# Optimization experiments

Hardware: AMD Instinct MI355X
Metric: run time of the kernel (lower is better)

The kernel has to match this reference:

```python
import jax, jax.numpy as jnp
import numpy as np

EPS = 1e-9

def setup_inputs() -> dict:
    key = jax.random.key(0)
    k1, k2 = jax.random.split(key)
    B, D = 65536, 512
    e = jax.random.normal(k1, (B, D), dtype=jnp.float32)
    tau = jax.random.normal(k2, (B, D), dtype=jnp.float32)
    return {"e": e, "tau": tau}

def reference(e, tau):
    # Barlow Twins (diagonal-only) loss.
    # torch .std(dim=0) is unbiased (ddof=1).
    B = e.shape[0]
    e_norm = (e - e.mean(axis=0)) / (e.std(axis=0, ddof=1) + EPS)
    tau_norm = (tau - tau.mean(axis=0)) / (tau.std(axis=0, ddof=1) + EPS)
    # diag(e_norm.T @ tau_norm) / B == per-feature batch reduction of products
    c_diag = jnp.sum(e_norm * tau_norm, axis=0) / B
    return jnp.sum((1.0 - c_diag) ** 2)
```

## Files before the change

kernel.cpp:

```cpp
#include <hip/hip_runtime.h>

#define BT_D  512
#define BT_D4 128
#define NBLK  1024
#define NTHR  256
#define BT_U  8

#define BT_ACC(ev, tv)                                                  \
    do {                                                                \
        se.x += (ev).x; se.y += (ev).y; se.z += (ev).z; se.w += (ev).w; \
        st.x += (tv).x; st.y += (tv).y; st.z += (tv).z; st.w += (tv).w; \
        se2.x = fmaf((ev).x, (ev).x, se2.x);                            \
        se2.y = fmaf((ev).y, (ev).y, se2.y);                            \
        se2.z = fmaf((ev).z, (ev).z, se2.z);                            \
        se2.w = fmaf((ev).w, (ev).w, se2.w);                            \
        st2.x = fmaf((tv).x, (tv).x, st2.x);                            \
        st2.y = fmaf((tv).y, (tv).y, st2.y);                            \
        st2.z = fmaf((tv).z, (tv).z, st2.z);                            \
        st2.w = fmaf((tv).w, (tv).w, st2.w);                            \
        set.x = fmaf((ev).x, (tv).x, set.x);                            \
        set.y = fmaf((ev).y, (tv).y, set.y);                            \
        set.z = fmaf((ev).z, (tv).z, set.z);                            \
        set.w = fmaf((ev).w, (tv).w, set.w);                            \
    } while (0)

__global__ __launch_bounds__(NTHR, 4) void bt_partial_kernel(
    const float4* __restrict__ e4, const float4* __restrict__ t4,
    float* __restrict__ acc, int B, int nslot)
{
    const int tid = threadIdx.x;
    const int c4  = tid & (BT_D4 - 1);
    const int r   = tid >> 7;

    float4 se  = make_float4(0.f, 0.f, 0.f, 0.f);
    float4 se2 = make_float4(0.f, 0.f, 0.f, 0.f);
    float4 st  = make_float4(0.f, 0.f, 0.f, 0.f);
    float4 st2 = make_float4(0.f, 0.f, 0.f, 0.f);
    float4 set = make_float4(0.f, 0.f, 0.f, 0.f);

    const size_t T  = (size_t)gridDim.x * NTHR;
    const size_t N4 = (size_t)B * BT_D4;
    size_t i = (size_t)blockIdx.x * NTHR + tid;

    for (; i + (BT_U - 1) * T < N4; i += BT_U * T) {
        float4 ev[BT_U], tv[BT_U];
#pragma unroll
        for (int u = 0; u < BT_U; ++u) {
            ev[u] = e4[i + u * T];
            tv[u] = t4[i + u * T];
        }
#pragma unroll
        for (int u = 0; u < BT_U; ++u) BT_ACC(ev[u], tv[u]);
    }
    for (; i < N4; i += T) {
        const float4 ev = e4[i];
        const float4 tv = t4[i];
        BT_ACC(ev, tv);
    }

    __shared__ float4 lds[BT_D4][5];
    if (r == 1) {
        lds[c4][0] = se;  lds[c4][1] = se2; lds[c4][2] = st;
        lds[c4][3] = st2; lds[c4][4] = set;
    }
    __syncthreads();
    if (r == 0) {
        float4 a;
        a = lds[c4][0]; se.x += a.x; se.y += a.y; se.z += a.z; se.w += a.w;
        a = lds[c4][1]; se2.x += a.x; se2.y += a.y; se2.z += a.z; se2.w += a.w;
        a = lds[c4][2]; st.x += a.x; st.y += a.y; st.z += a.z; st.w += a.w;
        a = lds[c4][3]; st2.x += a.x; st2.y += a.y; st2.z += a.z; st2.w += a.w;
        a = lds[c4][4]; set.x += a.x; set.y += a.y; set.z += a.z; set.w += a.w;

        float* ap = acc + (size_t)(blockIdx.x % nslot) * (5 * BT_D);
        const int col = c4 * 4;
        atomicAdd(&ap[0 * BT_D + col + 0], se.x);
        atomicAdd(&ap[0 * BT_D + col + 1], se.y);
        atomicAdd(&ap[0 * BT_D + col + 2], se.z);
        atomicAdd(&ap[0 * BT_D + col + 3], se.w);
        atomicAdd(&ap[1 * BT_D + col + 0], se2.x);
        atomicAdd(&ap[1 * BT_D + col + 1], se2.y);
        atomicAdd(&ap[1 * BT_D + col + 2], se2.z);
        atomicAdd(&ap[1 * BT_D + col + 3], se2.w);
        atomicAdd(&ap[2 * BT_D + col + 0], st.x);
        atomicAdd(&ap[2 * BT_D + col + 1], st.y);
        atomicAdd(&ap[2 * BT_D + col + 2], st.z);
        atomicAdd(&ap[2 * BT_D + col + 3], st.w);
        atomicAdd(&ap[3 * BT_D + col + 0], st2.x);
        atomicAdd(&ap[3 * BT_D + col + 1], st2.y);
        atomicAdd(&ap[3 * BT_D + col + 2], st2.z);
        atomicAdd(&ap[3 * BT_D + col + 3], st2.w);
        atomicAdd(&ap[4 * BT_D + col + 0], set.x);
        atomicAdd(&ap[4 * BT_D + col + 1], set.y);
        atomicAdd(&ap[4 * BT_D + col + 2], set.z);
        atomicAdd(&ap[4 * BT_D + col + 3], set.w);
    }
}

__global__ __launch_bounds__(512) void bt_final_kernel(
    const float* __restrict__ acc, float* __restrict__ out, int B, int nslot)
{
    const int d = threadIdx.x;
    double Se = 0, Se2 = 0, St = 0, St2 = 0, Set = 0;
    for (int s = 0; s < nslot; ++s) {
        const float* a = acc + (size_t)s * (5 * BT_D);
        Se  += a[0 * BT_D + d];
        Se2 += a[1 * BT_D + d];
        St  += a[2 * BT_D + d];
        St2 += a[3 * BT_D + d];
        Set += a[4 * BT_D + d];
    }
    const double Bd = (double)B;
    const double me = Se / Bd, mt = St / Bd;
    double ve = (Se2 - Bd * me * me) / (Bd - 1.0);
    double vt = (St2 - Bd * mt * mt) / (Bd - 1.0);
    ve = ve > 0.0 ? ve : 0.0;
    vt = vt > 0.0 ? vt : 0.0;
    const double sd_e = sqrt(ve) + 1e-9;
    const double sd_t = sqrt(vt) + 1e-9;
    const double c = (Set - Bd * me * mt) / (sd_e * sd_t * Bd);
    const double v = (1.0 - c) * (1.0 - c);

    __shared__ double red[BT_D];
    red[d] = v;
    __syncthreads();
    for (int s = BT_D / 2; s > 0; s >>= 1) {
        if (d < s) red[d] += red[d + s];
        __syncthreads();
    }
    if (d == 0) out[0] = (float)red[0];
}

extern "C" void kernel_launch(void* const* d_in, const int* in_sizes, int n_in,
                              void* d_out, int out_size, void* d_ws, size_t ws_size,
                              hipStream_t stream) {
    const float* e   = (const float*)d_in[0];
    const float* tau = (const float*)d_in[1];
    const int B = in_sizes[0] / BT_D;
    float* acc = (float*)d_ws;

    int nslot = 1;
    const size_t slot_bytes = (size_t)5 * BT_D * sizeof(float);
    if (ws_size >= 32 * slot_bytes)      nslot = 32;
    else if (ws_size >= 8 * slot_bytes)  nslot = 8;
    else if (ws_size >= 4 * slot_bytes)  nslot = 4;
    else if (ws_size >= 2 * slot_bytes)  nslot = 2;

    (void)hipMemsetAsync(d_ws, 0, (size_t)nslot * slot_bytes, stream);

    bt_partial_kernel<<<NBLK, NTHR, 0, stream>>>(
        (const float4*)e, (const float4*)tau, acc, B, nslot);
    bt_final_kernel<<<1, BT_D, 0, stream>>>(acc, (float*)d_out, B, nslot);
}
```

Baseline: 291.5 us.

## Stream inputs through LDS with async global_load_lds pipeline per wave

Replaces the grid-stride register loads with a per-wave software pipeline that uses global_load_lds to prefetch four stages of e and tau rows into shared memory, tracked with manual vmcnt waits. Each wave owns a contiguous range of rows and one half of the feature columns, which changes the access pattern to contiguous chunks. The final kernel is also restructured to read float4 slots across four thread groups and accumulate in float before converting to double. This adds reliance on inline waitcnt counting and clamped redundant loads at range ends, and the float accumulation in the final kernel may reduce precision.

```diff
diff --git a/kernel.cpp b/kernel.cpp
--- a/kernel.cpp
+++ b/kernel.cpp
@@ -1,10 +1,11 @@
 #include <hip/hip_runtime.h>
 
-#define BT_D  512
-#define BT_D4 128
-#define NBLK  1024
-#define NTHR  256
-#define BT_U  8
+#define BT_D   512
+#define BT_D4  128
+#define NBLK   1024
+#define NTHR   256
+#define NWAVE  4
+#define DEPTH  4
 
 #define BT_ACC(ev, tv)                                                  \
     do {                                                                \
@@ -24,13 +25,35 @@
         set.w = fmaf((ev).w, (tv).w, set.w);                            \
     } while (0)
 
+#define BT_ADD4(dst, a) \
+    do { (dst).x += (a).x; (dst).y += (a).y; (dst).z += (a).z; (dst).w += (a).w; } while (0)
+
+#define BT_ISSUE(sidx, slot_)                                                     \
+    do {                                                                          \
+        unsigned _p = p0 + (sidx);                                                \
+        if (_p >= pend) _p = pend - 1;    \
+        const unsigned _c = (_p << 1) | par;                                      \
+        const size_t _o = ((size_t)_c << 6) + (unsigned)lane;                     \
+        __builtin_amdgcn_global_load_lds(                                         \
+            (const __attribute__((address_space(1))) void*)(e4 + _o),            \
+            (__attribute__((address_space(3))) void*)&buf_e[w][slot_][0],        \
+            16, 0, 0);                                                            \
+        __builtin_amdgcn_global_load_lds(                                         \
+            (const __attribute__((address_space(1))) void*)(t4 + _o),            \
+            (__attribute__((address_space(3))) void*)&buf_t[w][slot_][0],        \
+            16, 0, 0);                                                            \
+    } while (0)
+
 __global__ __launch_bounds__(NTHR, 4) void bt_partial_kernel(
     const float4* __restrict__ e4, const float4* __restrict__ t4,
     float* __restrict__ acc, int B, int nslot)
 {
-    const int tid = threadIdx.x;
-    const int c4  = tid & (BT_D4 - 1);
-    const int r   = tid >> 7;
+    const int tid  = threadIdx.x;
+    const int w    = tid >> 6;
+    const int lane = tid & 63;
+
+    __shared__ float4 buf_e[NWAVE][DEPTH][64];
+    __shared__ float4 buf_t[NWAVE][DEPTH][64];
 
     float4 se  = make_float4(0.f, 0.f, 0.f, 0.f);
     float4 se2 = make_float4(0.f, 0.f, 0.f, 0.f);
@@ -38,42 +61,46 @@
     float4 st2 = make_float4(0.f, 0.f, 0.f, 0.f);
     float4 set = make_float4(0.f, 0.f, 0.f, 0.f);
 
-    const size_t T  = (size_t)gridDim.x * NTHR;
-    const size_t N4 = (size_t)B * BT_D4;
-    size_t i = (size_t)blockIdx.x * NTHR + tid;
-
-    for (; i + (BT_U - 1) * T < N4; i += BT_U * T) {
-        float4 ev[BT_U], tv[BT_U];
-#pragma unroll
-        for (int u = 0; u < BT_U; ++u) {
-            ev[u] = e4[i + u * T];
-            tv[u] = t4[i + u * T];
+    const unsigned npair  = (unsigned)B;
+    const unsigned wg     = (unsigned)blockIdx.x * NWAVE + w;
+    const unsigned par    = wg & 1u;
+    const unsigned pairid = wg >> 1;
+    const unsigned PW     = (NBLK * NWAVE) >> 1;
+    const unsigned cpw    = (npair + PW - 1) / PW;
+    const unsigned p0     = pairid * cpw;
+    const unsigned pend   = (p0 + cpw < npair) ? (p0 + cpw) : npair;
+
+    if (p0 < pend) {
+        const unsigned steps = pend - p0;
+        BT_ISSUE(0u, 0); BT_ISSUE(1u, 1); BT_ISSUE(2u, 2); BT_ISSUE(3u, 3);
+        for (unsigned s = 0; s < steps; ++s) {
+            const unsigned slot = s & (DEPTH - 1);
+            asm volatile("s_waitcnt vmcnt(6)" ::: "memory");
+            const float4 ev = buf_e[w][slot][lane];
+            const float4 tv = buf_t[w][slot][lane];
+            asm volatile("" ::: "memory");
+            BT_ISSUE(s + DEPTH, slot);
+            BT_ACC(ev, tv);
         }
-#pragma unroll
-        for (int u = 0; u < BT_U; ++u) BT_ACC(ev[u], tv[u]);
-    }
-    for (; i < N4; i += T) {
-        const float4 ev = e4[i];
-        const float4 tv = t4[i];
-        BT_ACC(ev, tv);
-    }
-
-    __shared__ float4 lds[BT_D4][5];
-    if (r == 1) {
-        lds[c4][0] = se;  lds[c4][1] = se2; lds[c4][2] = st;
-        lds[c4][3] = st2; lds[c4][4] = set;
-    }
-    __syncthreads();
-    if (r == 0) {
-        float4 a;
-        a = lds[c4][0]; se.x += a.x; se.y += a.y; se.z += a.z; se.w += a.w;
-        a = lds[c4][1]; se2.x += a.x; se2.y += a.y; se2.z += a.z; se2.w += a.w;
-        a = lds[c4][2]; st.x += a.x; st.y += a.y; st.z += a.z; st.w += a.w;
-        a = lds[c4][3]; st2.x += a.x; st2.y += a.y; st2.z += a.z; st2.w += a.w;
-        a = lds[c4][4]; set.x += a.x; set.y += a.y; set.z += a.z; set.w += a.w;
-
-        float* ap = acc + (size_t)(blockIdx.x % nslot) * (5 * BT_D);
-        const int col = c4 * 4;
+    }
+    asm volatile("s_waitcnt vmcnt(0)" ::: "memory");
+    __syncthreads();
+
+    float4 (*scr)[5] = (float4 (*)[5])&buf_e[0][0][0];
+    if (w >= 2) {
+        float4 (*L)[5] = scr + (w - 2) * 64;
+        L[lane][0] = se;  L[lane][1] = se2; L[lane][2] = st;
+        L[lane][3] = st2; L[lane][4] = set;
+    }
+    __syncthreads();
+    if (w < 2) {
+        float4 (*L)[5] = scr + w * 64;
+        BT_ADD4(se,  L[lane][0]); BT_ADD4(se2, L[lane][1]);
+        BT_ADD4(st,  L[lane][2]); BT_ADD4(st2, L[lane][3]);
+        BT_ADD4(set, L[lane][4]);
+
+        float* ap = acc + (size_t)(blockIdx.x & (nslot - 1)) * (5 * BT_D);
+        const int col = (lane + (w << 6)) * 4;
         atomicAdd(&ap[0 * BT_D + col + 0], se.x);
         atomicAdd(&ap[0 * BT_D + col + 1], se.y);
         atomicAdd(&ap[0 * BT_D + col + 2], se.z);
@@ -97,38 +124,68 @@
     }
 }
 
+#define BT_FIN(Se_, Se2_, St_, St2_, Set_)                               \
+    do {                                                                 \
+        const double Se = (Se_), Se2 = (Se2_), St = (St_), St2 = (St2_), \
+                     Set = (Set_);                                       \
+        const double me = Se / Bd, mt = St / Bd;                         \
+        double ve = (Se2 - Bd * me * me) / (Bd - 1.0);                   \
+        double vt = (St2 - Bd * mt * mt) / (Bd - 1.0);                   \
+        ve = ve > 0.0 ? ve : 0.0;                                        \
+        vt = vt > 0.0 ? vt : 0.0;                                        \
+        const double sd_e = sqrt(ve) + 1e-9;                             \
+        const double sd_t = sqrt(vt) + 1e-9;                             \
+        const double c = (Set - Bd * me * mt) / (sd_e * sd_t * Bd);      \
+        vsum += (1.0 - c) * (1.0 - c);                                   \
+    } while (0)
+
 __global__ __launch_bounds__(512) void bt_final_kernel(
     const float* __restrict__ acc, float* __restrict__ out, int B, int nslot)
 {
-    const int d = threadIdx.x;
-    double Se = 0, Se2 = 0, St = 0, St2 = 0, Set = 0;
-    for (int s = 0; s < nslot; ++s) {
-        const float* a = acc + (size_t)s * (5 * BT_D);
-        Se  += a[0 * BT_D + d];
-        Se2 += a[1 * BT_D + d];
-        St  += a[2 * BT_D + d];
-        St2 += a[3 * BT_D + d];
-        Set += a[4 * BT_D + d];
-    }
-    const double Bd = (double)B;
-    const double me = Se / Bd, mt = St / Bd;
-    double ve = (Se2 - Bd * me * me) / (Bd - 1.0);
-    double vt = (St2 - Bd * mt * mt) / (Bd - 1.0);
-    ve = ve > 0.0 ? ve : 0.0;
-    vt = vt > 0.0 ? vt : 0.0;
-    const double sd_e = sqrt(ve) + 1e-9;
-    const double sd_t = sqrt(vt) + 1e-9;
-    const double c = (Set - Bd * me * mt) / (sd_e * sd_t * Bd);
-    const double v = (1.0 - c) * (1.0 - c);
-
-    __shared__ double red[BT_D];
-    red[d] = v;
-    __syncthreads();
-    for (int s = BT_D / 2; s > 0; s >>= 1) {
-        if (d < s) red[d] += red[d + s];
+    const int t  = threadIdx.x;
+    const int c4 = t & 127;
+    const int q  = t >> 7;
+
+    float4 S0 = make_float4(0.f, 0.f, 0.f, 0.f);
+    float4 S1 = S0, S2 = S0, S3 = S0, S4 = S0;
+    const float4* a4 = (const float4*)acc;
+    for (int s = q; s < nslot; s += 4) {
+        const float4* a = a4 + (size_t)s * (5 * BT_D4);
+        float4 x;
+        x = a[0 * BT_D4 + c4]; BT_ADD4(S0, x);
+        x = a[1 * BT_D4 + c4]; BT_ADD4(S1, x);
+        x = a[2 * BT_D4 + c4]; BT_ADD4(S2, x);
+        x = a[3 * BT_D4 + c4]; BT_ADD4(S3, x);
+        x = a[4 * BT_D4 + c4]; BT_ADD4(S4, x);
+    }
+
+    __shared__ float4 L[3][128][5];
+    __shared__ double R[128];
+    if (q) {
+        L[q - 1][c4][0] = S0; L[q - 1][c4][1] = S1; L[q - 1][c4][2] = S2;
+        L[q - 1][c4][3] = S3; L[q - 1][c4][4] = S4;
+    }
+    __syncthreads();
+    if (q == 0) {
+        for (int j = 0; j < 3; ++j) {
+            BT_ADD4(S0, L[j][c4][0]); BT_ADD4(S1, L[j][c4][1]);
+            BT_ADD4(S2, L[j][c4][2]); BT_ADD4(S3, L[j][c4][3]);
+            BT_ADD4(S4, L[j][c4][4]);
+        }
+        const double Bd = (double)B;
+        double vsum = 0.0;
+        BT_FIN(S0.x, S1.x, S2.x, S3.x, S4.x);
+        BT_FIN(S0.y, S1.y, S2.y, S3.y, S4.y);
+        BT_FIN(S0.z, S1.z, S2.z, S3.z, S4.z);
+        BT_FIN(S0.w, S1.w, S2.w, S3.w, S4.w);
+        R[c4] = vsum;
+    }
+    __syncthreads();
+    for (int s2 = 64; s2 > 0; s2 >>= 1) {
+        if (t < s2) R[t] += R[t + s2];
         __syncthreads();
     }
-    if (d == 0) out[0] = (float)red[0];
+    if (t == 0) out[0] = (float)R[0];
 }
 
 extern "C" void kernel_launch(void* const* d_in, const int* in_sizes, int n_in,
@@ -150,5 +207,5 @@
 
     bt_partial_kernel<<<NBLK, NTHR, 0, stream>>>(
         (const float4*)e, (const float4*)tau, acc, B, nslot);
-    bt_final_kernel<<<1, BT_D, 0, stream>>>(acc, (float*)d_out, B, nslot);
+    bt_final_kernel<<<1, 512, 0, stream>>>(acc, (float*)d_out, B, nslot);
 }
```

Measured after the change: 308.9 us. 6.0% more time.
